# Performance work log

Hardware: AMD Instinct MI355X
Metric: run time of the kernel (lower is better)

## Reference

```python
import jax, jax.numpy as jnp
import numpy as np

PHI = 1.6
JITTER = 1e-4
ETA = 1.0
BETA = 0.5
EPS_CHOL = 1e-6
R_NEIGH = 2


def _solve3(L, d):
    # lower-triangular 3x3 forward substitution; L broadcasts against d[..., 3]
    y0 = d[..., 0] / L[..., 0, 0]
    y1 = (d[..., 1] - L[..., 1, 0] * y0) / L[..., 1, 1]
    y2 = (d[..., 2] - L[..., 2, 0] * y0 - L[..., 2, 1] * y1) / L[..., 2, 2]
    return jnp.stack([y0, y1, y2], axis=-1)


def _overlap_score(delta, L):
    # fused_gaussian_overlap_score: Gaussian log-overlap ~ -0.5*(Mahalanobis + logdet)
    y = _solve3(L, delta)
    maha = jnp.sum(y * y, axis=-1)
    logdet = 2.0 * jnp.sum(jnp.log(jnp.diagonal(L, axis1=-2, axis2=-1)), axis=-1)
    return -0.5 * (maha + logdet)


def _head(x, ln_g, ln_b, W1, b1, W2, b2):
    # LayerNorm -> Linear -> SiLU -> Linear(->1), squeeze
    m = jnp.mean(x, axis=-1, keepdims=True)
    v = jnp.var(x, axis=-1, keepdims=True)
    h = (x - m) / jnp.sqrt(v + 1e-5) * ln_g + ln_b
    h = jax.nn.silu(h @ W1 + b1)
    return (h @ W2 + b2)[..., 0]


def setup_inputs() -> dict:
    key = jax.random.key(0)
    ks = jax.random.split(key, 12)
    B, Kp, M, C = 2, 1024, 8, 256
    s_parent = jax.random.normal(ks[0], (B, Kp, C), jnp.float32)
    mu_p = jax.random.normal(ks[1], (B, Kp, 3), jnp.float32) * 10.0
    A = jax.random.normal(ks[2], (B, Kp, 3, 3), jnp.float32) * 0.5
    Sigma_p = jnp.einsum('bkij,bklj->bkil', A, A) + 0.05 * jnp.eye(3, dtype=jnp.float32)
    mask_parent = jnp.ones((B, Kp), jnp.float32)
    xi_noise = jax.random.normal(ks[3], (B, Kp, M, 3), jnp.float32)
    emb = jax.random.normal(ks[4], (M, C), jnp.float32) * 0.02
    lin = lambda k, fi, fo, s=0.02: jax.random.normal(k, (fi, fo), jnp.float32) * s
    return dict(
        s_parent=s_parent, mu_p=mu_p, Sigma_p=Sigma_p, mask_parent=mask_parent,
        xi_noise=xi_noise, emb=emb,
        gate_ln_g=jnp.ones((C,), jnp.float32), gate_ln_b=jnp.zeros((C,), jnp.float32),
        gate_W1=lin(ks[5], C, C), gate_b1=jnp.zeros((C,), jnp.float32),
        gate_W2=lin(ks[6], C, 1), gate_b2=jnp.zeros((1,), jnp.float32),
        prior_ln_g=jnp.ones((C,), jnp.float32), prior_ln_b=jnp.zeros((C,), jnp.float32),
        prior_W1=lin(ks[7], C, C), prior_b1=jnp.zeros((C,), jnp.float32),
        prior_W2=lin(ks[8], C, 1), prior_b2=jnp.zeros((1,), jnp.float32),
        geom_W=lin(ks[9], C, 3, 0.01), geom_b=jnp.zeros((3,), jnp.float32),
        K_target=6144,
    )


def reference(s_parent, mu_p, Sigma_p, mask_parent, xi_noise, emb,
              gate_ln_g, gate_ln_b, gate_W1, gate_b1, gate_W2, gate_b2,
              prior_ln_g, prior_ln_b, prior_W1, prior_b1, prior_W2, prior_b2,
              geom_W, geom_b, K_target):
    B, Kp, C = s_parent.shape
    M = emb.shape[0]
    Kc = Kp * M
    I3 = jnp.eye(3, dtype=s_parent.dtype)

    # --- candidate children from per-parent Cholesky splat ---
    Lp = jnp.linalg.cholesky(Sigma_p + EPS_CHOL * I3)               # [B,Kp,3,3]
    xi = xi_noise + (emb @ geom_W + geom_b)                          # [B,Kp,M,3]
    mu0 = mu_p[:, :, None, :] + jnp.einsum('bkae,bkme->bkma', Lp, xi)
    mu0 = mu0.reshape(B, Kc, 3)

    j0 = jnp.repeat(jnp.arange(Kp), M)                               # [Kc] birth parent
    t_ids = jnp.tile(jnp.arange(M), Kp)                              # [Kc] child slot
    m0 = mask_parent[:, j0]

    # --- gate g ---
    gate_in = s_parent[:, j0, :] + emb[t_ids]                        # [B,Kc,C]
    b = _head(gate_in, gate_ln_g, gate_ln_b, gate_W1, gate_b1, gate_W2, gate_b2)
    a = jax.nn.softplus(_head(s_parent, prior_ln_g, prior_ln_b, prior_W1, prior_b1, prior_W2, prior_b2))
    b = b + BETA * jnp.log(a[:, j0] + 1e-8)
    g = jax.nn.sigmoid(b / max(ETA, 1e-6)) * m0                      # [B,Kc]
    loss_count = jnp.mean((jnp.sum(g, axis=1) - float(K_target)) ** 2)

    # --- top-R neighbor parents by overlap score (indices only, no grad) ---
    mu0_birth = mu_p[:, j0, :]                                       # mu of birth parent
    delta1 = mu0_birth[:, :, None, :] - mu_p[:, None, :, :]          # [B,Kc,Kp,3]
    score1 = _overlap_score(delta1, Lp[:, None])                     # [B,Kc,Kp]
    self_hot = (jnp.arange(Kp)[None, :] == j0[:, None])              # [Kc,Kp]
    score1 = jnp.where(self_hot[None], 1e9, score1)
    _, neigh = jax.lax.top_k(jax.lax.stop_gradient(score1), R_NEIGH) # [B,Kc,R], col0=j0

    bidx = jnp.arange(B)[:, None, None]
    mu_nei = mu_p[bidx, neigh]                                       # [B,Kc,R,3]
    Sig_nei = Sigma_p[bidx, neigh]                                   # [B,Kc,R,3,3]
    L_nei = Lp[bidx, neigh]
    s_nei = s_parent[bidx, neigh]                                    # [B,Kc,R,C]

    # --- soft responsibilities over the R neighbors ---
    score2 = _overlap_score(mu0[:, :, None, :] - mu_nei, L_nei)      # [B,Kc,R]
    w = jax.nn.softmax(score2, axis=-1)

    # --- moment-matching refine (sparse form of B_resp: rows of B are w scattered at neigh) ---
    mu_child = jnp.einsum('bir,bird->bid', w, mu_nei)                # [B,Kc,3]
    intra = jnp.einsum('bir,birmn->bimn', w, Sig_nei) * PHI ** (-2)
    dmu = mu_nei - mu_child[:, :, None, :]
    inter = jnp.einsum('bir,birm,birn->bimn', w, dmu, dmu)
    Sigma_child = intra + inter + JITTER * I3                        # [B,Kc,3,3]

    s_mix = jnp.einsum('bir,birc->bic', w, s_nei)
    s_child0 = g[..., None] * s_mix                                  # [B,Kc,C]
    return s_child0, mu_child, Sigma_child, g, loss_count
```

## Files before the change

### kernel.cpp

```cpp
#include <hip/hip_runtime.h>
#include <math.h>

#define NPAR 2048
#define KP   1024
#define MM   8
#define CC   256
#define KC   8192
#define NCH  16384

#define WS_PKL    0
#define WS_PKI    8192
#define WS_PKM    16384
#define WS_L22    24576
#define WS_MEANSP 26624
#define WS_SUMSQ  28672
#define WS_DOT8   30720
#define WS_APRIOR 47104
#define WS_EGATE  49152
#define WS_UGATE  51200
#define WS_C0GATE 51456
#define WS_GEO    51712
#define WS_MEANE  51736
#define WS_SUMSQE 51744
#define WS_NEIGH  51752
#define WS_PGATE  53824

#define OUT_S    0
#define OUT_MU   4194304
#define OUT_SIG  4243456
#define OUT_G    4390912
#define OUT_LOSS 4407296

__device__ __forceinline__ float siluf(float x){ return x / (1.f + expf(-x)); }
__device__ __forceinline__ float softplusf(float x){ return x > 20.f ? x : log1pf(expf(x)); }

template<int NR>
__device__ __forceinline__ void gemm_k(const float* __restrict__ W1, int t,
                                       const float xs[][256], float* acc) {
  float wn[8];
#pragma unroll
  for (int i = 0; i < 8; i++) wn[i] = W1[i * 256 + t];
  for (int kb = 0; kb < 256; kb += 8) {
    float wc[8];
#pragma unroll
    for (int i = 0; i < 8; i++) wc[i] = wn[i];
    if (kb + 8 < 256) {
#pragma unroll
      for (int i = 0; i < 8; i++) wn[i] = W1[(kb + 8 + i) * 256 + t];
    }
#pragma unroll
    for (int i = 0; i < 8; i += 4) {
#pragma unroll
      for (int r = 0; r < NR; r++) {
        float4 x = *(const float4*)&xs[r][kb + i];
        acc[r] += x.x * wc[i] + x.y * wc[i+1] + x.z * wc[i+2] + x.w * wc[i+3];
      }
    }
  }
}

__global__ __launch_bounds__(256) void kP1(const float* __restrict__ sp,
                                           const float* __restrict__ mu_p,
                                           const float* __restrict__ Sig,
                                           const float* __restrict__ emb,
                                           const float* __restrict__ geom_W,
                                           const float* __restrict__ geom_b,
                                           float* __restrict__ ws) {
  int blk = blockIdx.x;
  int t = threadIdx.x;
  if (blk < 512) {
    int pid  = blk * 4 + (t >> 6);
    int lane = t & 63;
    const float4 v = *(const float4*)(sp + pid * CC + lane * 4);
    float s  = v.x + v.y + v.z + v.w;
    float ss = v.x*v.x + v.y*v.y + v.z*v.z + v.w*v.w;
    float pd[8];
#pragma unroll
    for (int m = 0; m < 8; m++) {
      float4 e = *(const float4*)(emb + m * CC + lane * 4);
      pd[m] = v.x*e.x + v.y*e.y + v.z*e.z + v.w*e.w;
    }
#pragma unroll
    for (int o = 32; o > 0; o >>= 1) {
      s  += __shfl_xor(s, o);
      ss += __shfl_xor(ss, o);
#pragma unroll
      for (int m = 0; m < 8; m++) pd[m] += __shfl_xor(pd[m], o);
    }
    if (lane == 0) {
      ws[WS_MEANSP + pid] = s * (1.f / 256.f);
      ws[WS_SUMSQ + pid]  = ss;
#pragma unroll
      for (int m = 0; m < 8; m++) ws[WS_DOT8 + pid * 8 + m] = pd[m];
    }
  } else if (blk < 520) {
    int pid = (blk - 512) * 256 + t;
    const float* S = Sig + pid * 9;
    float a00 = S[0] + 1e-6f, a10 = S[3], a11 = S[4] + 1e-6f;
    float a20 = S[6], a21 = S[7], a22 = S[8] + 1e-6f;
    float L00 = sqrtf(a00); float i0 = 1.f / L00;
    float L10 = a10 * i0, L20 = a20 * i0;
    float L11 = sqrtf(a11 - L10 * L10); float i1 = 1.f / L11;
    float L21 = (a21 - L20 * L10) * i1;
    float L22 = sqrtf(a22 - L20 * L20 - L21 * L21); float i2 = 1.f / L22;
    float logdet = 2.f * logf(L00 * L11 * L22);
    float4 pkl = {L10, L20, L21, logdet};
    float4 pki = {i0, i1, i2, L00};
    float4 pkm = {mu_p[pid*3+0], mu_p[pid*3+1], mu_p[pid*3+2], L11};
    *(float4*)(ws + WS_PKL + pid * 4) = pkl;
    *(float4*)(ws + WS_PKI + pid * 4) = pki;
    *(float4*)(ws + WS_PKM + pid * 4) = pkm;
    ws[WS_L22 + pid] = L22;
  } else {
    if (t < 192) {
      int o = t >> 3, lane8 = t & 7;
      int m = o / 3, d = o % 3;
      float acc = 0.f;
      for (int k = lane8; k < 256; k += 8) acc += emb[m * 256 + k] * geom_W[k * 3 + d];
      acc += __shfl_xor(acc, 1); acc += __shfl_xor(acc, 2); acc += __shfl_xor(acc, 4);
      if (lane8 == 0) ws[WS_GEO + o] = acc + geom_b[d];
    } else {
      int o = (t - 192) >> 3, lane8 = t & 7;
      if (o < 8) {
        float s = 0.f, ss = 0.f;
        for (int k = lane8; k < 256; k += 8) { float e = emb[o * 256 + k]; s += e; ss += e * e; }
        s  += __shfl_xor(s, 1);  s  += __shfl_xor(s, 2);  s  += __shfl_xor(s, 4);
        ss += __shfl_xor(ss, 1); ss += __shfl_xor(ss, 2); ss += __shfl_xor(ss, 4);
        if (lane8 == 0) { ws[WS_MEANE + o] = s * (1.f / 256.f); ws[WS_SUMSQE + o] = ss; }
      }
    }
  }
}

__global__ __launch_bounds__(256) void kP2(const float* __restrict__ sp,
                                           const float* __restrict__ emb,
                                           const float* __restrict__ g_ln_g,
                                           const float* __restrict__ g_ln_b,
                                           const float* __restrict__ gW1,
                                           const float* __restrict__ gb1,
                                           const float* __restrict__ p_ln_g,
                                           const float* __restrict__ p_ln_b,
                                           const float* __restrict__ pW1,
                                           const float* __restrict__ pb1,
                                           const float* __restrict__ pW2,
                                           const float* __restrict__ pb2,
                                           float* __restrict__ ws) {
  __shared__ float xs[18][256];
  __shared__ float red[4][16];
  int blk = blockIdx.x;
  int t = threadIdx.x;

  if (blk < 512) {
    int wv = blk * 4 + (t >> 6);
    int lane = t & 63;
    int b = wv >> 10;
    int j = wv & (KP - 1);
    const float4 qm = *(const float4*)(ws + WS_PKM + wv * 4);
    float qx = qm.x, qy = qm.y, qz = qm.z;
    float best = -3.4e38f; int bidx = 1 << 30;
    for (int it = 0; it < 16; it++) {
      int k = it * 64 + lane;
      int idx = b * KP + k;
      float4 pl = *(const float4*)(ws + WS_PKL + idx * 4);
      float4 pi = *(const float4*)(ws + WS_PKI + idx * 4);
      float4 pm = *(const float4*)(ws + WS_PKM + idx * 4);
      float dx = qx - pm.x, dy = qy - pm.y, dz = qz - pm.z;
      float y0 = dx * pi.x;
      float y1 = (dy - pl.x * y0) * pi.y;
      float y2 = (dz - pl.y * y0 - pl.z * y1) * pi.z;
      float sc = -0.5f * (y0*y0 + y1*y1 + y2*y2 + pl.w);
      if (k == j) sc = -3.4e38f;
      if (sc > best || (sc == best && k < bidx)) { best = sc; bidx = k; }
    }
#pragma unroll
    for (int o = 32; o > 0; o >>= 1) {
      float ob = __shfl_xor(best, o);
      int   oi = __shfl_xor(bidx, o);
      if (ob > best || (ob == best && oi < bidx)) { best = ob; bidx = oi; }
    }
    if (lane == 0) ((int*)ws)[WS_NEIGH + wv] = bidx;
  } else if (blk < 640) {
    int base = (blk - 512) * 16;
    float lg = g_ln_g[t];
#pragma unroll
    for (int r = 0; r < 16; r++) xs[r][t] = sp[(base + r) * 256 + t] * lg;
    __syncthreads();
    float acc[16];
#pragma unroll
    for (int r = 0; r < 16; r++) acc[r] = 0.f;
    gemm_k<16>(gW1, t, xs, acc);
#pragma unroll
    for (int r = 0; r < 16; r++) ws[WS_PGATE + (base + r) * 256 + t] = acc[r];
  } else if (blk < 768) {
    int base = (blk - 640) * 16;
    float lp = p_ln_g[t];
#pragma unroll
    for (int r = 0; r < 16; r++) xs[r][t] = sp[(base + r) * 256 + t] * lp;
    xs[16][t] = lp;
    xs[17][t] = p_ln_b[t];
    __syncthreads();
    float acc[18];
#pragma unroll
    for (int r = 0; r < 18; r++) acc[r] = 0.f;
    gemm_k<18>(pW1, t, xs, acc);

    float up  = acc[16];
    float c0p = acc[17] + pb1[t];
    float w2 = pW2[t];
    float tv[16];
#pragma unroll
    for (int r = 0; r < 16; r++) {
      float mean = ws[WS_MEANSP + base + r];
      float var  = ws[WS_SUMSQ + base + r] * (1.f / 256.f) - mean * mean;
      float rstd = rsqrtf(var + 1e-5f);
      float h = (acc[r] - mean * up) * rstd + c0p;
      tv[r] = siluf(h) * w2;
    }
#pragma unroll
    for (int o = 32; o > 0; o >>= 1) {
#pragma unroll
      for (int r = 0; r < 16; r++) tv[r] += __shfl_xor(tv[r], o);
    }
    int wave = t >> 6;
    if ((t & 63) == 0) {
#pragma unroll
      for (int r = 0; r < 16; r++) red[wave][r] = tv[r];
    }
    __syncthreads();
    if (t < 16) {
      float sum = red[0][t] + red[1][t] + red[2][t] + red[3][t] + pb2[0];
      ws[WS_APRIOR + base + t] = softplusf(sum);
    }
  } else {
    float lg = g_ln_g[t];
#pragma unroll
    for (int r = 0; r < 8; r++) xs[r][t] = emb[r * 256 + t] * lg;
    xs[8][t] = lg;
    xs[9][t] = g_ln_b[t];
    __syncthreads();
    float acc[10];
#pragma unroll
    for (int r = 0; r < 10; r++) acc[r] = 0.f;
    gemm_k<10>(gW1, t, xs, acc);
#pragma unroll
    for (int r = 0; r < 8; r++) ws[WS_EGATE + r * 256 + t] = acc[r];
    ws[WS_UGATE + t]  = acc[8];
    ws[WS_C0GATE + t] = acc[9] + gb1[t];
  }
}

__global__ __launch_bounds__(256) void kD(const float* __restrict__ sp,
                                          const float* __restrict__ Sig,
                                          const float* __restrict__ mask,
                                          const float* __restrict__ xi_noise,
                                          const float* __restrict__ gW2,
                                          const float* __restrict__ gb2,
                                          const float* __restrict__ ws,
                                          float* __restrict__ out) {
  int wv   = blockIdx.x * 4 + (threadIdx.x >> 6);
  int lane = threadIdx.x & 63;
  int b = wv >> 13;
  int i = wv & (KC - 1);
  int j = i >> 3;
  int m = i & 7;
  int prow = b * KP + j;

  float mean_x = ws[WS_MEANSP + prow] + ws[WS_MEANE + m];
  float Ex2 = ws[WS_SUMSQ + prow] + 2.f * ws[WS_DOT8 + prow * 8 + m] + ws[WS_SUMSQE + m];
  float var = Ex2 * (1.f / 256.f) - mean_x * mean_x;
  float rstd = rsqrtf(var + 1e-5f);

  int c4 = lane * 4;
  float Pv[4], Ev[4], Uv[4], C0v[4], W2v[4];
  *(float4*)Pv  = *(const float4*)(ws + WS_PGATE + prow * 256 + c4);
  *(float4*)Ev  = *(const float4*)(ws + WS_EGATE + m * 256 + c4);
  *(float4*)Uv  = *(const float4*)(ws + WS_UGATE + c4);
  *(float4*)C0v = *(const float4*)(ws + WS_C0GATE + c4);
  *(float4*)W2v = *(const float4*)(gW2 + c4);
  float partial = 0.f;
#pragma unroll
  for (int q = 0; q < 4; q++) {
    float pre = (Pv[q] + Ev[q] - mean_x * Uv[q]) * rstd + C0v[q];
    partial += siluf(pre) * W2v[q];
  }
#pragma unroll
  for (int o = 32; o > 0; o >>= 1) partial += __shfl_xor(partial, o);
  float aP = ws[WS_APRIOR + prow];
  float bval = partial + gb2[0] + 0.5f * logf(aP + 1e-8f);
  float g = (1.f / (1.f + expf(-bval))) * mask[prow];

  const float4 plP = *(const float4*)(ws + WS_PKL + prow * 4);
  const float4 piP = *(const float4*)(ws + WS_PKI + prow * 4);
  const float4 pmP = *(const float4*)(ws + WS_PKM + prow * 4);
  float L22 = ws[WS_L22 + prow];

  int xbase = (prow * 8 + m) * 3;
  float x0 = xi_noise[xbase + 0] + ws[WS_GEO + m * 3 + 0];
  float x1 = xi_noise[xbase + 1] + ws[WS_GEO + m * 3 + 1];
  float x2 = xi_noise[xbase + 2] + ws[WS_GEO + m * 3 + 2];
  float m0x = pmP.x + piP.w * x0;
  float m0y = pmP.y + plP.x * x0 + pmP.w * x1;
  float m0z = pmP.z + plP.y * x0 + plP.z * x1 + L22 * x2;

  int n1 = ((const int*)ws)[WS_NEIGH + prow];
  int nrow1 = b * KP + n1;
  const float4 plN = *(const float4*)(ws + WS_PKL + nrow1 * 4);
  const float4 piN = *(const float4*)(ws + WS_PKI + nrow1 * 4);
  const float4 pmN = *(const float4*)(ws + WS_PKM + nrow1 * 4);

  float sc[2], nx[2], ny[2], nz[2];
  {
    float dx = m0x - pmP.x, dy = m0y - pmP.y, dz = m0z - pmP.z;
    float y0 = dx * piP.x;
    float y1 = (dy - plP.x * y0) * piP.y;
    float y2 = (dz - plP.y * y0 - plP.z * y1) * piP.z;
    sc[0] = -0.5f * (y0*y0 + y1*y1 + y2*y2 + plP.w);
    nx[0] = pmP.x; ny[0] = pmP.y; nz[0] = pmP.z;
  }
  {
    float dx = m0x - pmN.x, dy = m0y - pmN.y, dz = m0z - pmN.z;
    float y0 = dx * piN.x;
    float y1 = (dy - plN.x * y0) * piN.y;
    float y2 = (dz - plN.y * y0 - plN.z * y1) * piN.z;
    sc[1] = -0.5f * (y0*y0 + y1*y1 + y2*y2 + plN.w);
    nx[1] = pmN.x; ny[1] = pmN.y; nz[1] = pmN.z;
  }
  float mxs = fmaxf(sc[0], sc[1]);
  float e0 = expf(sc[0] - mxs), e1 = expf(sc[1] - mxs);
  float inv = 1.f / (e0 + e1);
  float w0 = e0 * inv, w1 = e1 * inv;

  float mcx = w0 * nx[0] + w1 * nx[1];
  float mcy = w0 * ny[0] + w1 * ny[1];
  float mcz = w0 * nz[0] + w1 * nz[1];

  float d0x = nx[0] - mcx, d0y = ny[0] - mcy, d0z = nz[0] - mcz;
  float d1x = nx[1] - mcx, d1y = ny[1] - mcy, d1z = nz[1] - mcz;
  const float* S0 = Sig + prow * 9;
  const float* S1 = Sig + nrow1 * 9;
  const float PHIm2 = 0.390625f;
  float Sout[9];
  float dd0[3] = {d0x, d0y, d0z};
  float dd1[3] = {d1x, d1y, d1z};
#pragma unroll
  for (int a = 0; a < 3; a++)
#pragma unroll
    for (int e = 0; e < 3; e++) {
      float v = (w0 * S0[a*3+e] + w1 * S1[a*3+e]) * PHIm2
              + w0 * dd0[a] * dd0[e] + w1 * dd1[a] * dd1[e];
      if (a == e) v += 1e-4f;
      Sout[a*3+e] = v;
    }

  if (lane == 0) {
    float* om = out + OUT_MU + wv * 3;
    om[0] = mcx; om[1] = mcy; om[2] = mcz;
    out[OUT_G + wv] = g;
    float* os = out + OUT_SIG + wv * 9;
#pragma unroll
    for (int q = 0; q < 9; q++) os[q] = Sout[q];
  }

  float s0v[4], s1v[4], ov[4];
  *(float4*)s0v = *(const float4*)(sp + prow * 256 + c4);
  *(float4*)s1v = *(const float4*)(sp + nrow1 * 256 + c4);
  float gw0 = g * w0, gw1 = g * w1;
#pragma unroll
  for (int q = 0; q < 4; q++) ov[q] = gw0 * s0v[q] + gw1 * s1v[q];
  *(float4*)(out + OUT_S + wv * 256 + c4) = *(float4*)ov;
}

__global__ __launch_bounds__(256) void kF(const float* __restrict__ out_in,
                                          const int* __restrict__ Kt,
                                          float* __restrict__ out) {
  __shared__ float red[4][2];
  int t = threadIdx.x;
  const float* gp = out_in + OUT_G;
  float s0 = 0.f, s1 = 0.f;
  for (int it = 0; it < 32; it++) {
    s0 += gp[it * 256 + t];
    s1 += gp[KC + it * 256 + t];
  }
#pragma unroll
  for (int o = 32; o > 0; o >>= 1) {
    s0 += __shfl_xor(s0, o);
    s1 += __shfl_xor(s1, o);
  }
  int wave = t >> 6;
  if ((t & 63) == 0) { red[wave][0] = s0; red[wave][1] = s1; }
  __syncthreads();
  if (t == 0) {
    float S0 = red[0][0] + red[1][0] + red[2][0] + red[3][0];
    float S1 = red[0][1] + red[1][1] + red[2][1] + red[3][1];
    float K = (float)Kt[0];
    float l0 = S0 - K, l1 = S1 - K;
    out[OUT_LOSS] = 0.5f * (l0 * l0 + l1 * l1);
  }
}

extern "C" void kernel_launch(void* const* d_in, const int* in_sizes, int n_in,
                              void* d_out, int out_size, void* d_ws, size_t ws_size,
                              hipStream_t stream) {
  const float* s_parent   = (const float*)d_in[0];
  const float* mu_p       = (const float*)d_in[1];
  const float* Sigma_p    = (const float*)d_in[2];
  const float* mask_par   = (const float*)d_in[3];
  const float* xi_noise   = (const float*)d_in[4];
  const float* emb        = (const float*)d_in[5];
  const float* gate_ln_g  = (const float*)d_in[6];
  const float* gate_ln_b  = (const float*)d_in[7];
  const float* gate_W1    = (const float*)d_in[8];
  const float* gate_b1    = (const float*)d_in[9];
  const float* gate_W2    = (const float*)d_in[10];
  const float* gate_b2    = (const float*)d_in[11];
  const float* prior_ln_g = (const float*)d_in[12];
  const float* prior_ln_b = (const float*)d_in[13];
  const float* prior_W1   = (const float*)d_in[14];
  const float* prior_b1   = (const float*)d_in[15];
  const float* prior_W2   = (const float*)d_in[16];
  const float* prior_b2   = (const float*)d_in[17];
  const float* geom_W     = (const float*)d_in[18];
  const float* geom_b     = (const float*)d_in[19];
  const int*   K_target   = (const int*)d_in[20];

  float* ws  = (float*)d_ws;
  float* out = (float*)d_out;

  kP1<<<521, 256, 0, stream>>>(s_parent, mu_p, Sigma_p, emb, geom_W, geom_b, ws);
  kP2<<<769, 256, 0, stream>>>(s_parent, emb, gate_ln_g, gate_ln_b, gate_W1, gate_b1,
                               prior_ln_g, prior_ln_b, prior_W1, prior_b1,
                               prior_W2, prior_b2, ws);
  kD<<<NCH / 4, 256, 0, stream>>>(s_parent, Sigma_p, mask_par, xi_noise,
                                  gate_W2, gate_b2, ws, out);
  kF<<<1, 256, 0, stream>>>(out, K_target, out);
}
```

Before: 163.2 us.

## Split parent GEMMs along K into four partial slices and move prior head to kD

```diff
diff --git a/kernel.cpp b/kernel.cpp
--- a/kernel.cpp
+++ b/kernel.cpp
@@ -15,7 +15,6 @@
 #define WS_MEANSP 26624
 #define WS_SUMSQ  28672
 #define WS_DOT8   30720
-#define WS_APRIOR 47104
 #define WS_EGATE  49152
 #define WS_UGATE  51200
 #define WS_C0GATE 51456
@@ -23,7 +22,10 @@
 #define WS_MEANE  51736
 #define WS_SUMSQE 51744
 #define WS_NEIGH  51752
-#define WS_PGATE  53824
+#define WS_UPRI   53824
+#define WS_C0PRI  54080
+#define WS_PG     54336
+#define WS_PP     2151488
 
 #define OUT_S    0
 #define OUT_MU   4194304
@@ -142,11 +144,8 @@
                                            const float* __restrict__ p_ln_b,
                                            const float* __restrict__ pW1,
                                            const float* __restrict__ pb1,
-                                           const float* __restrict__ pW2,
-                                           const float* __restrict__ pb2,
                                            float* __restrict__ ws) {
-  __shared__ float xs[18][256];
-  __shared__ float red[4][16];
+  __shared__ float xs[10][256];
   int blk = blockIdx.x;
   int t = threadIdx.x;
 
@@ -179,59 +178,49 @@
       if (ob > best || (ob == best && oi < bidx)) { best = ob; bidx = oi; }
     }
     if (lane == 0) ((int*)ws)[WS_NEIGH + wv] = bidx;
-  } else if (blk < 640) {
-    int base = (blk - 512) * 16;
-    float lg = g_ln_g[t];
-#pragma unroll
-    for (int r = 0; r < 16; r++) xs[r][t] = sp[(base + r) * 256 + t] * lg;
+  } else if (blk < 2560) {
+    int idx = blk - 512;
+    bool isGate = idx < 1024;
+    int q2 = isGate ? idx : idx - 1024;
+    const float* W1 = isGate ? gW1 : pW1;
+    const float* ln = isGate ? g_ln_g : p_ln_g;
+    int dst = isGate ? WS_PG : WS_PP;
+    int rb = q2 >> 2, s = q2 & 3;
+    int base = rb * 8, k0 = s * 64;
+    float (*xs8)[64] = (float(*)[64])&xs[0][0];
+#pragma unroll
+    for (int u = 0; u < 2; u++) {
+      int e = t + 256 * u;
+      int r = e >> 6, kk = e & 63;
+      xs8[r][kk] = sp[(base + r) * 256 + k0 + kk] * ln[k0 + kk];
+    }
     __syncthreads();
-    float acc[16];
-#pragma unroll
-    for (int r = 0; r < 16; r++) acc[r] = 0.f;
-    gemm_k<16>(gW1, t, xs, acc);
-#pragma unroll
-    for (int r = 0; r < 16; r++) ws[WS_PGATE + (base + r) * 256 + t] = acc[r];
-  } else if (blk < 768) {
-    int base = (blk - 640) * 16;
-    float lp = p_ln_g[t];
-#pragma unroll
-    for (int r = 0; r < 16; r++) xs[r][t] = sp[(base + r) * 256 + t] * lp;
-    xs[16][t] = lp;
-    xs[17][t] = p_ln_b[t];
-    __syncthreads();
-    float acc[18];
-#pragma unroll
-    for (int r = 0; r < 18; r++) acc[r] = 0.f;
-    gemm_k<18>(pW1, t, xs, acc);
-
-    float up  = acc[16];
-    float c0p = acc[17] + pb1[t];
-    float w2 = pW2[t];
-    float tv[16];
-#pragma unroll
-    for (int r = 0; r < 16; r++) {
-      float mean = ws[WS_MEANSP + base + r];
-      float var  = ws[WS_SUMSQ + base + r] * (1.f / 256.f) - mean * mean;
-      float rstd = rsqrtf(var + 1e-5f);
-      float h = (acc[r] - mean * up) * rstd + c0p;
-      tv[r] = siluf(h) * w2;
-    }
-#pragma unroll
-    for (int o = 32; o > 0; o >>= 1) {
-#pragma unroll
-      for (int r = 0; r < 16; r++) tv[r] += __shfl_xor(tv[r], o);
-    }
-    int wave = t >> 6;
-    if ((t & 63) == 0) {
-#pragma unroll
-      for (int r = 0; r < 16; r++) red[wave][r] = tv[r];
-    }
-    __syncthreads();
-    if (t < 16) {
-      float sum = red[0][t] + red[1][t] + red[2][t] + red[3][t] + pb2[0];
-      ws[WS_APRIOR + base + t] = softplusf(sum);
-    }
-  } else {
+    const float* W = W1 + k0 * 256;
+    float acc[8] = {0,0,0,0,0,0,0,0};
+    float wn[8];
+#pragma unroll
+    for (int i = 0; i < 8; i++) wn[i] = W[i * 256 + t];
+    for (int kb = 0; kb < 64; kb += 8) {
+      float wc[8];
+#pragma unroll
+      for (int i = 0; i < 8; i++) wc[i] = wn[i];
+      if (kb + 8 < 64) {
+#pragma unroll
+        for (int i = 0; i < 8; i++) wn[i] = W[(kb + 8 + i) * 256 + t];
+      }
+#pragma unroll
+      for (int i = 0; i < 8; i += 4) {
+#pragma unroll
+        for (int r = 0; r < 8; r++) {
+          float4 x = *(const float4*)&xs8[r][kb + i];
+          acc[r] += x.x * wc[i] + x.y * wc[i+1] + x.z * wc[i+2] + x.w * wc[i+3];
+        }
+      }
+    }
+#pragma unroll
+    for (int r = 0; r < 8; r++)
+      ws[dst + ((base + r) * 4 + s) * 256 + t] = acc[r];
+  } else if (blk == 2560) {
     float lg = g_ln_g[t];
 #pragma unroll
     for (int r = 0; r < 8; r++) xs[r][t] = emb[r * 256 + t] * lg;
@@ -246,6 +235,14 @@
     for (int r = 0; r < 8; r++) ws[WS_EGATE + r * 256 + t] = acc[r];
     ws[WS_UGATE + t]  = acc[8];
     ws[WS_C0GATE + t] = acc[9] + gb1[t];
+  } else {
+    xs[0][t] = p_ln_g[t];
+    xs[1][t] = p_ln_b[t];
+    __syncthreads();
+    float acc[2] = {0.f, 0.f};
+    gemm_k<2>(pW1, t, xs, acc);
+    ws[WS_UPRI  + t] = acc[0];
+    ws[WS_C0PRI + t] = acc[1] + pb1[t];
   }
 }
 
@@ -255,6 +252,8 @@
                                           const float* __restrict__ xi_noise,
                                           const float* __restrict__ gW2,
                                           const float* __restrict__ gb2,
+                                          const float* __restrict__ pW2,
+                                          const float* __restrict__ pb2,
                                           const float* __restrict__ ws,
                                           float* __restrict__ out) {
   int wv   = blockIdx.x * 4 + (threadIdx.x >> 6);
@@ -264,15 +263,46 @@
   int j = i >> 3;
   int m = i & 7;
   int prow = b * KP + j;
-
-  float mean_x = ws[WS_MEANSP + prow] + ws[WS_MEANE + m];
+  int c4 = lane * 4;
+
+  float meanP = ws[WS_MEANSP + prow];
+  float varP  = ws[WS_SUMSQ + prow] * (1.f / 256.f) - meanP * meanP;
+  float rstdP = rsqrtf(varP + 1e-5f);
+
+  float PPv[4] = {0,0,0,0};
+#pragma unroll
+  for (int s = 0; s < 4; s++) {
+    float4 pp = *(const float4*)(ws + WS_PP + ((prow * 4 + s) << 8) + c4);
+    PPv[0] += pp.x; PPv[1] += pp.y; PPv[2] += pp.z; PPv[3] += pp.w;
+  }
+  float4 upv  = *(const float4*)(ws + WS_UPRI + c4);
+  float4 c0pv = *(const float4*)(ws + WS_C0PRI + c4);
+  float4 w2pv = *(const float4*)(pW2 + c4);
+  float upr[4]  = {upv.x, upv.y, upv.z, upv.w};
+  float c0pr[4] = {c0pv.x, c0pv.y, c0pv.z, c0pv.w};
+  float w2pr[4] = {w2pv.x, w2pv.y, w2pv.z, w2pv.w};
+  float psum = 0.f;
+#pragma unroll
+  for (int q = 0; q < 4; q++) {
+    float h = (PPv[q] - meanP * upr[q]) * rstdP + c0pr[q];
+    psum += siluf(h) * w2pr[q];
+  }
+#pragma unroll
+  for (int o = 32; o > 0; o >>= 1) psum += __shfl_xor(psum, o);
+  float aP = softplusf(psum + pb2[0]);
+
+  float mean_x = meanP + ws[WS_MEANE + m];
   float Ex2 = ws[WS_SUMSQ + prow] + 2.f * ws[WS_DOT8 + prow * 8 + m] + ws[WS_SUMSQE + m];
   float var = Ex2 * (1.f / 256.f) - mean_x * mean_x;
   float rstd = rsqrtf(var + 1e-5f);
 
-  int c4 = lane * 4;
-  float Pv[4], Ev[4], Uv[4], C0v[4], W2v[4];
-  *(float4*)Pv  = *(const float4*)(ws + WS_PGATE + prow * 256 + c4);
+  float Pv[4] = {0,0,0,0};
+#pragma unroll
+  for (int s = 0; s < 4; s++) {
+    float4 pg = *(const float4*)(ws + WS_PG + ((prow * 4 + s) << 8) + c4);
+    Pv[0] += pg.x; Pv[1] += pg.y; Pv[2] += pg.z; Pv[3] += pg.w;
+  }
+  float Ev[4], Uv[4], C0v[4], W2v[4];
   *(float4*)Ev  = *(const float4*)(ws + WS_EGATE + m * 256 + c4);
   *(float4*)Uv  = *(const float4*)(ws + WS_UGATE + c4);
   *(float4*)C0v = *(const float4*)(ws + WS_C0GATE + c4);
@@ -285,7 +315,6 @@
   }
 #pragma unroll
   for (int o = 32; o > 0; o >>= 1) partial += __shfl_xor(partial, o);
-  float aP = ws[WS_APRIOR + prow];
   float bval = partial + gb2[0] + 0.5f * logf(aP + 1e-8f);
   float g = (1.f / (1.f + expf(-bval))) * mask[prow];
 
@@ -427,10 +456,9 @@
   float* out = (float*)d_out;
 
   kP1<<<521, 256, 0, stream>>>(s_parent, mu_p, Sigma_p, emb, geom_W, geom_b, ws);
-  kP2<<<769, 256, 0, stream>>>(s_parent, emb, gate_ln_g, gate_ln_b, gate_W1, gate_b1,
-                               prior_ln_g, prior_ln_b, prior_W1, prior_b1,
-                               prior_W2, prior_b2, ws);
+  kP2<<<2562, 256, 0, stream>>>(s_parent, emb, gate_ln_g, gate_ln_b, gate_W1, gate_b1,
+                                prior_ln_g, prior_ln_b, prior_W1, prior_b1, ws);
   kD<<<NCH / 4, 256, 0, stream>>>(s_parent, Sigma_p, mask_par, xi_noise,
-                                  gate_W2, gate_b2, ws, out);
+                                  gate_W2, gate_b2, prior_W2, prior_b2, ws, out);
   kF<<<1, 256, 0, stream>>>(out, K_target, out);
 }
```

Measured after the change: 162.2 us. No clear change (-0.6%).
